# Kernel tuning notes

Hardware: AMD Instinct MI355X
Metric: run time of the kernel (lower is better)

The kernel has to match this reference:

```python
import math
import jax, jax.numpy as jnp
import numpy as np

B, N, D = 4, 1024, 512
HEADS, K = 8, 3
DH = D // HEADS
SMAX, SMIN, ALPHA_S = 0.2, 0.8, 3.0


def setup_inputs() -> dict:
    key = jax.random.key(0)
    ks = jax.random.split(key, 6)
    X = jax.random.normal(ks[0], (B, N, D), dtype=jnp.float32)
    # per-head GraphConstructor temperature (init 1.0 in torch)
    temperature = jnp.ones((HEADS,), dtype=jnp.float32)
    # per-head, per-hop filter weights: [HEADS, K+1, DH, DH]
    W_filt = jax.random.normal(ks[1], (HEADS, K + 1, DH, DH), dtype=jnp.float32) / math.sqrt(DH)
    # per-head hop mixing coefficients (random so output is non-trivial)
    alpha = jax.random.normal(ks[2], (HEADS, K + 1), dtype=jnp.float32) * 0.5
    W_proj = jax.random.normal(ks[3], (D, D), dtype=jnp.float32) / math.sqrt(D)
    b_proj = jnp.zeros((D,), dtype=jnp.float32)
    return {"X": X, "temperature": temperature, "W_filt": W_filt, "alpha": alpha,
            "W_proj": W_proj, "b_proj": b_proj, "layer_idx": 1, "L": 4}


def reference(X, temperature, W_filt, alpha, W_proj, b_proj, layer_idx, L):
    b, n, d = X.shape
    Xh = X.reshape(b, n, HEADS, DH).transpose(0, 2, 1, 3)  # [B,H,N,DH]

    # sparsity schedule -> static top-k size
    sparsity = SMIN + (SMAX - SMIN) * math.exp(-ALPHA_S * layer_idx / L)
    k_val = max(1, int((1.0 - sparsity) * n))

    tau = jnp.clip(temperature, 0.1, 5.0)  # [H]
    scale = math.sqrt(DH)
    # per-head attention scores: [B,H,N,N]
    S = jnp.einsum('bhnd,bhmd->bhnm', Xh, Xh) / (scale * tau[None, :, None, None])

    if k_val < n:
        thresh = jax.lax.top_k(S, k_val)[0][..., -1:]  # k-th largest per row
        S = jnp.where(S < thresh, -jnp.inf, S)
    A = jax.nn.softmax(S, axis=-1)  # row-stochastic sparse-pattern adjacency

    # K-hop polynomial filter, all heads at once
    P = Xh
    H = alpha[None, :, 0, None, None] * jnp.einsum('bhnd,hde->bhne', P, W_filt[:, 0])
    for k in range(1, K + 1):
        P = jnp.einsum('bhnm,bhmd->bhnd', A, P)
        H = H + alpha[None, :, k, None, None] * jnp.einsum('bhnd,hde->bhne', P, W_filt[:, k])

    out = H.transpose(0, 2, 1, 3).reshape(b, n, d)  # concat heads
    return out @ W_proj.T + b_proj
```

## Files before the change

### kernel.cpp

```cpp
#include <hip/hip_runtime.h>
#include <math.h>

#define Nq   1024
#define Dq   512
#define Hq   8
#define KH   3
#define DHq  64
#define NBH  32

typedef __attribute__((ext_vector_type(8))) __bf16 bf16x8;
typedef __attribute__((ext_vector_type(4))) float f32x4;

#define LDA 136
#define LDW 72


__device__ __forceinline__ unsigned short f2bf(float f) {
    unsigned int u = __float_as_uint(f);
    u += 0x7FFFu + ((u >> 16) & 1u);
    return (unsigned short)(u >> 16);
}
__device__ __forceinline__ float bf2f(unsigned short b) {
    return __uint_as_float(((unsigned int)b) << 16);
}
__device__ __forceinline__ unsigned key16(unsigned int b) {
    return (b & 0x8000u) ? (0xFFFFu & ~b) : (b | 0x8000u);
}
__device__ __forceinline__ uint2 pack4(float4 v) {
    return make_uint2((unsigned)f2bf(v.x) | ((unsigned)f2bf(v.y) << 16),
                      (unsigned)f2bf(v.z) | ((unsigned)f2bf(v.w) << 16));
}
__device__ __forceinline__ f32x4 fzero() { f32x4 z = {0.f, 0.f, 0.f, 0.f}; return z; }



__global__ __launch_bounds__(256) void xcast_kernel(const float* __restrict__ X,
                                                    unsigned short* __restrict__ Xn,
                                                    unsigned short* __restrict__ Xt) {
    __shared__ float T[64][68];
    int tid = threadIdx.x;
    int bh = blockIdx.y, b = bh >> 3, h = bh & 7;
    int n0 = blockIdx.x << 6;
    const float* Xg = X + ((size_t)b * Nq + n0) * Dq + h * DHq;
#pragma unroll
    for (int u = 0; u < 4; ++u) {
        int idx = tid + (u << 8);
        int r = idx >> 4, c4 = (idx & 15) << 2;
        float4 v = *(const float4*)&Xg[(size_t)r * Dq + c4];
        *(uint2*)&Xn[((size_t)bh * Nq + n0 + r) * DHq + c4] = pack4(v);
        T[c4 + 0][r] = v.x; T[c4 + 1][r] = v.y; T[c4 + 2][r] = v.z; T[c4 + 3][r] = v.w;
    }
    __syncthreads();
#pragma unroll
    for (int u = 0; u < 4; ++u) {
        int idx = tid + (u << 8);
        int d = idx >> 4, n4 = (idx & 15) << 2;
        float4 v = make_float4(T[d][n4], T[d][n4 + 1], T[d][n4 + 2], T[d][n4 + 3]);
        *(uint2*)&Xt[((size_t)bh * DHq + d) * Nq + n0 + n4] = pack4(v);
    }
}

__global__ __launch_bounds__(256) void score_mfma(const unsigned short* __restrict__ Xn,
                                                  const float* __restrict__ temperature,
                                                  unsigned short* __restrict__ Sbf) {
    __shared__ unsigned short Xi[64 * LDW], Xj[64 * LDW];
    int tid = threadIdx.x, lane = tid & 63, w = tid >> 6;
    int bh = blockIdx.z, i0 = blockIdx.y << 6, j0 = blockIdx.x << 6;
    const unsigned short* Xb = Xn + (size_t)bh * Nq * DHq;
    {
        int row = tid >> 3, o = (tid & 7) << 3;
#pragma unroll
        for (int u = 0; u < 2; ++u) {
            int r = row + (u << 5);
            *(uint4*)&Xi[r * LDW + o] = *(const uint4*)&Xb[(size_t)(i0 + r) * DHq + o];
            *(uint4*)&Xj[r * LDW + o] = *(const uint4*)&Xb[(size_t)(j0 + r) * DHq + o];
        }
    }
    __syncthreads();
    f32x4 acc[4] = {fzero(), fzero(), fzero(), fzero()};
    int brow = lane & 15, ko = (lane >> 4) << 3;
    const unsigned short* Afr = &Xi[((w << 4) + brow) * LDW + ko];
#pragma unroll
    for (int ks = 0; ks < 2; ++ks) {
        bf16x8 af = *(const bf16x8*)(Afr + (ks << 5));
#pragma unroll
        for (int nt = 0; nt < 4; ++nt) {
            bf16x8 bfv = *(const bf16x8*)&Xj[((nt << 4) + brow) * LDW + (ks << 5) + ko];
            acc[nt] = __builtin_amdgcn_mfma_f32_16x16x32_bf16(af, bfv, acc[nt], 0, 0, 0);
        }
    }
    float tau = fminf(fmaxf(temperature[bh & 7], 0.1f), 5.0f);
    float inv = 1.0f / (8.0f * tau);
    int nrow = (w << 4) + ((lane >> 4) << 2);
    unsigned short* Sp = Sbf + ((size_t)bh * Nq + i0 + nrow) * Nq + j0;
#pragma unroll
    for (int nt = 0; nt < 4; ++nt)
#pragma unroll
        for (int r = 0; r < 4; ++r)
            Sp[(size_t)r * Nq + (nt << 4) + brow] = f2bf(acc[nt][r] * inv);
}

__global__ __launch_bounds__(256) void topk_softmax_kernel(unsigned short* __restrict__ Sbf,
                                                           const int* __restrict__ layer_idx,
                                                           const int* __restrict__ Lptr) {
    int tid = threadIdx.x;
    int w = tid >> 6, lane = tid & 63;
    unsigned short* Srow = Sbf + ((size_t)blockIdx.x * 4 + w) * Nq;
    uint4 q0 = ((const uint4*)Srow)[lane * 2];
    uint4 q1 = ((const uint4*)Srow)[lane * 2 + 1];
    float v[16]; unsigned int k16[16];
    {
        unsigned int ww[8] = {q0.x, q0.y, q0.z, q0.w, q1.x, q1.y, q1.z, q1.w};
#pragma unroll
        for (int i = 0; i < 8; ++i) {
            unsigned lo16 = ww[i] & 0xFFFFu, hi16 = ww[i] >> 16;
            v[2 * i]     = __uint_as_float(lo16 << 16);
            v[2 * i + 1] = __uint_as_float(hi16 << 16);
            k16[2 * i]     = key16(lo16);
            k16[2 * i + 1] = key16(hi16);
        }
    }

    double sp = 0.8 + (0.2 - 0.8) * exp(-3.0 * (double)layer_idx[0] / (double)Lptr[0]);
    int kv = (int)((1.0 - sp) * (double)Nq);
    if (kv < 1) kv = 1;

    unsigned int tk = 0;
    if (kv < Nq) {
        unsigned int lo = 0;
#pragma unroll
        for (int bit = 15; bit >= 0; --bit) {
            unsigned int t = lo | (1u << bit);
            int cnt = 0;
#pragma unroll
            for (int i = 0; i < 16; ++i)
                cnt += (int)__popcll(__ballot(k16[i] >= t));
            if (cnt >= kv) lo = t;
        }
        tk = lo;
    }

    float m = v[0];
#pragma unroll
    for (int i = 1; i < 16; ++i) m = fmaxf(m, v[i]);
#pragma unroll
    for (int off = 32; off; off >>= 1) m = fmaxf(m, __shfl_xor(m, off));
    float sum = 0.f;
#pragma unroll
    for (int i = 0; i < 16; ++i) {
        float e = (k16[i] >= tk) ? __expf(v[i] - m) : 0.0f;
        v[i] = e; sum += e;
    }
#pragma unroll
    for (int off = 32; off; off >>= 1) sum += __shfl_xor(sum, off);
    float inv = 1.0f / sum;
    unsigned int ow[8];
#pragma unroll
    for (int i = 0; i < 8; ++i)
        ow[i] = (unsigned)f2bf(v[2 * i] * inv) | ((unsigned)f2bf(v[2 * i + 1] * inv) << 16);
    ((uint4*)Srow)[lane * 2]     = make_uint4(ow[0], ow[1], ow[2], ow[3]);
    ((uint4*)Srow)[lane * 2 + 1] = make_uint4(ow[4], ow[5], ow[6], ow[7]);
}

__global__ __launch_bounds__(256) void filt0_mfma(const unsigned short* __restrict__ Xn,
                                                  const float* __restrict__ W_filt,
                                                  const float* __restrict__ alpha,
                                                  float* __restrict__ Hacc) {
    __shared__ unsigned short PnL[64 * LDW], WtL[64 * LDW];
    int tid = threadIdx.x, lane = tid & 63, w = tid >> 6;
    int bh = blockIdx.y, b = bh >> 3, h = bh & 7;
    int n0 = blockIdx.x << 6;
    {
        int row = tid >> 3, o = (tid & 7) << 3;
        const unsigned short* Xb = Xn + ((size_t)bh * Nq + n0) * DHq;
#pragma unroll
        for (int u = 0; u < 2; ++u) {
            int r = row + (u << 5);
            *(uint4*)&PnL[r * LDW + o] = *(const uint4*)&Xb[(size_t)r * DHq + o];
        }
    }
    const float* Wg = W_filt + (size_t)h * (KH + 1) * DHq * DHq;
    for (int u = tid; u < 1024; u += 256) {
        int d = u >> 4, e4 = (u & 15) << 2;
        float4 wv = *(const float4*)&Wg[d * 64 + e4];
        WtL[(e4 + 0) * LDW + d] = f2bf(wv.x);
        WtL[(e4 + 1) * LDW + d] = f2bf(wv.y);
        WtL[(e4 + 2) * LDW + d] = f2bf(wv.z);
        WtL[(e4 + 3) * LDW + d] = f2bf(wv.w);
    }
    __syncthreads();
    f32x4 acc[4] = {fzero(), fzero(), fzero(), fzero()};
    int brow = lane & 15, ko = (lane >> 4) << 3;
    const unsigned short* Afr = &PnL[((w << 4) + brow) * LDW + ko];
#pragma unroll
    for (int ks = 0; ks < 2; ++ks) {
        bf16x8 af = *(const bf16x8*)(Afr + (ks << 5));
#pragma unroll
        for (int nt = 0; nt < 4; ++nt) {
            bf16x8 bfv = *(const bf16x8*)&WtL[((nt << 4) + brow) * LDW + (ks << 5) + ko];
            acc[nt] = __builtin_amdgcn_mfma_f32_16x16x32_bf16(af, bfv, acc[nt], 0, 0, 0);
        }
    }
    float av = alpha[h * (KH + 1)];
    int nrow = (w << 4) + ((lane >> 4) << 2);
    float* Ho = Hacc + ((size_t)b * Nq + n0 + nrow) * Dq + h * DHq;
#pragma unroll
    for (int nt = 0; nt < 4; ++nt)
#pragma unroll
        for (int r = 0; r < 4; ++r)
            Ho[(size_t)r * Dq + (nt << 4) + brow] = av * acc[nt][r];
}

__global__ __launch_bounds__(256) void apf_mfma(const unsigned short* __restrict__ Abf,
                                                const unsigned short* __restrict__ Ptin,
                                                unsigned short* __restrict__ Ptout, int writeP,
                                                const float* __restrict__ W_filt,
                                                const float* __restrict__ alpha,
                                                float* __restrict__ Hacc, int khop) {
    __shared__ unsigned short A_lds[2][64 * LDA];
    __shared__ unsigned short P_lds[2][64 * LDA];
    int tid = threadIdx.x, lane = tid & 63, w = tid >> 6;
    int bh = blockIdx.y, b = bh >> 3, h = bh & 7;
    int n0 = blockIdx.x << 6;
    const unsigned short* Ag = Abf + ((size_t)bh * Nq + n0) * Nq;
    const unsigned short* Pg = Ptin + (size_t)bh * DHq * Nq;
    int r0 = tid >> 4, oo = (tid & 15) << 3;

    uint4 ra[4], rp[4];
#pragma unroll
    for (int u = 0; u < 4; ++u) {
        ra[u] = *(const uint4*)&Ag[(size_t)(r0 + (u << 4)) * Nq + oo];
        rp[u] = *(const uint4*)&Pg[(size_t)(r0 + (u << 4)) * Nq + oo];
    }
#pragma unroll
    for (int u = 0; u < 4; ++u) {
        *(uint4*)&A_lds[0][(r0 + (u << 4)) * LDA + oo] = ra[u];
        *(uint4*)&P_lds[0][(r0 + (u << 4)) * LDA + oo] = rp[u];
    }
    __syncthreads();

    f32x4 acc[4] = {fzero(), fzero(), fzero(), fzero()};
    int brow = lane & 15, ko = (lane >> 4) << 3;
    int cur = 0;

    for (int kt = 0; kt < 8; ++kt) {
        if (kt < 7) {
            int j = (kt + 1) << 7;
#pragma unroll
            for (int u = 0; u < 4; ++u) {
                ra[u] = *(const uint4*)&Ag[(size_t)(r0 + (u << 4)) * Nq + j + oo];
                rp[u] = *(const uint4*)&Pg[(size_t)(r0 + (u << 4)) * Nq + j + oo];
            }
        }
        const unsigned short* Afr = &A_lds[cur][((w << 4) + brow) * LDA + ko];
#pragma unroll
        for (int ks = 0; ks < 4; ++ks) {
            bf16x8 af = *(const bf16x8*)(Afr + (ks << 5));
#pragma unroll
            for (int nt = 0; nt < 4; ++nt) {
                bf16x8 bfv = *(const bf16x8*)&P_lds[cur][((nt << 4) + brow) * LDA + (ks << 5) + ko];
                acc[nt] = __builtin_amdgcn_mfma_f32_16x16x32_bf16(af, bfv, acc[nt], 0, 0, 0);
            }
        }
        if (kt < 7) {
#pragma unroll
            for (int u = 0; u < 4; ++u) {
                *(uint4*)&A_lds[cur ^ 1][(r0 + (u << 4)) * LDA + oo] = ra[u];
                *(uint4*)&P_lds[cur ^ 1][(r0 + (u << 4)) * LDA + oo] = rp[u];
            }
        }
        __syncthreads();
        cur ^= 1;
    }

    int nrow = (w << 4) + ((lane >> 4) << 2);
    int dcol = lane & 15;
    if (writeP) {
#pragma unroll
        for (int nt = 0; nt < 4; ++nt) {
            uint2 pk = make_uint2(
                (unsigned)f2bf(acc[nt][0]) | ((unsigned)f2bf(acc[nt][1]) << 16),
                (unsigned)f2bf(acc[nt][2]) | ((unsigned)f2bf(acc[nt][3]) << 16));
            *(uint2*)&Ptout[(size_t)bh * DHq * Nq + (size_t)((nt << 4) + dcol) * Nq + n0 + nrow] = pk;
        }
    }
    unsigned short* PnL = &A_lds[0][0];
    unsigned short* WtL = &P_lds[0][0];
#pragma unroll
    for (int nt = 0; nt < 4; ++nt)
#pragma unroll
        for (int r = 0; r < 4; ++r)
            PnL[(nrow + r) * LDW + (nt << 4) + dcol] = f2bf(acc[nt][r]);
    const float* Wg = W_filt + ((size_t)h * (KH + 1) + khop) * DHq * DHq;
    for (int u = tid; u < 1024; u += 256) {
        int d = u >> 4, e4 = (u & 15) << 2;
        float4 wv = *(const float4*)&Wg[d * 64 + e4];
        WtL[(e4 + 0) * LDW + d] = f2bf(wv.x);
        WtL[(e4 + 1) * LDW + d] = f2bf(wv.y);
        WtL[(e4 + 2) * LDW + d] = f2bf(wv.z);
        WtL[(e4 + 3) * LDW + d] = f2bf(wv.w);
    }
    __syncthreads();
    f32x4 hacc[4] = {fzero(), fzero(), fzero(), fzero()};
    const unsigned short* Pfr = &PnL[((w << 4) + brow) * LDW + ko];
#pragma unroll
    for (int ks = 0; ks < 2; ++ks) {
        bf16x8 af = *(const bf16x8*)(Pfr + (ks << 5));
#pragma unroll
        for (int nt = 0; nt < 4; ++nt) {
            bf16x8 bfv = *(const bf16x8*)&WtL[((nt << 4) + brow) * LDW + (ks << 5) + ko];
            hacc[nt] = __builtin_amdgcn_mfma_f32_16x16x32_bf16(af, bfv, hacc[nt], 0, 0, 0);
        }
    }
    float av = alpha[h * (KH + 1) + khop];
    float* Ho = Hacc + ((size_t)b * Nq + n0 + nrow) * Dq + h * DHq;
#pragma unroll
    for (int nt = 0; nt < 4; ++nt)
#pragma unroll
        for (int r = 0; r < 4; ++r) {
            float* p = Ho + (size_t)r * Dq + (nt << 4) + dcol;
            *p += av * hacc[nt][r];
        }
}

__global__ __launch_bounds__(256) void proj_mfma(const float* __restrict__ Hacc,
                                                 const float* __restrict__ Wp,
                                                 const float* __restrict__ bp,
                                                 float* __restrict__ out) {
    __shared__ unsigned short Hl[64 * LDA], Wl[64 * LDA];
    int tid = threadIdx.x, lane = tid & 63, w = tid >> 6;
    int i0 = blockIdx.y << 6, j0 = blockIdx.x << 6;
    f32x4 acc[4] = {fzero(), fzero(), fzero(), fzero()};
    int brow = lane & 15, ko = (lane >> 4) << 3;
    for (int kt = 0; kt < 4; ++kt) {
#pragma unroll
        for (int u = 0; u < 8; ++u) {
            int c = tid + (u << 8);
            int r = c >> 5, o4 = (c & 31) << 2;
            float4 hv = *(const float4*)&Hacc[(size_t)(i0 + r) * Dq + (kt << 7) + o4];
            *(uint2*)&Hl[r * LDA + o4] = pack4(hv);
            float4 wv = *(const float4*)&Wp[(size_t)(j0 + r) * Dq + (kt << 7) + o4];
            *(uint2*)&Wl[r * LDA + o4] = pack4(wv);
        }
        __syncthreads();
        const unsigned short* Afr = &Hl[((w << 4) + brow) * LDA + ko];
#pragma unroll
        for (int ks = 0; ks < 4; ++ks) {
            bf16x8 af = *(const bf16x8*)(Afr + (ks << 5));
#pragma unroll
            for (int nt = 0; nt < 4; ++nt) {
                bf16x8 bfv = *(const bf16x8*)&Wl[((nt << 4) + brow) * LDA + (ks << 5) + ko];
                acc[nt] = __builtin_amdgcn_mfma_f32_16x16x32_bf16(af, bfv, acc[nt], 0, 0, 0);
            }
        }
        __syncthreads();
    }
    int nrow = (w << 4) + ((lane >> 4) << 2);
#pragma unroll
    for (int nt = 0; nt < 4; ++nt) {
        float bb = bp[j0 + (nt << 4) + brow];
#pragma unroll
        for (int r = 0; r < 4; ++r)
            out[(size_t)(i0 + nrow + r) * Dq + j0 + (nt << 4) + brow] = acc[nt][r] + bb;
    }
}


extern "C" void kernel_launch(void* const* d_in, const int* in_sizes, int n_in,
                              void* d_out, int out_size, void* d_ws, size_t ws_size,
                              hipStream_t stream) {
    (void)in_sizes; (void)n_in; (void)out_size; (void)ws_size;
    const float* X           = (const float*)d_in[0];
    const float* temperature = (const float*)d_in[1];
    const float* W_filt      = (const float*)d_in[2];
    const float* alpha       = (const float*)d_in[3];
    const float* W_proj      = (const float*)d_in[4];
    const float* b_proj      = (const float*)d_in[5];
    const int*   layer_idx   = (const int*)d_in[6];
    const int*   Lp          = (const int*)d_in[7];
    float* out = (float*)d_out;

    unsigned short* Sbf = (unsigned short*)d_ws;
    unsigned short* Xn  = Sbf + (size_t)NBH * Nq * Nq;
    unsigned short* Xt  = Xn  + (size_t)NBH * Nq * DHq;
    unsigned short* Pt1 = Xt  + (size_t)NBH * DHq * Nq;
    unsigned short* Pt2 = Pt1 + (size_t)NBH * DHq * Nq;
    float* Hacc = (float*)(Pt2 + (size_t)NBH * DHq * Nq);

    dim3 blk(256);
    xcast_kernel<<<dim3(16, 32), blk, 0, stream>>>(X, Xn, Xt);
    score_mfma<<<dim3(16, 16, 32), blk, 0, stream>>>(Xn, temperature, Sbf);
    topk_softmax_kernel<<<dim3(NBH * Nq / 4), blk, 0, stream>>>(Sbf, layer_idx, Lp);

    filt0_mfma<<<dim3(16, 32), blk, 0, stream>>>(Xn, W_filt, alpha, Hacc);
    apf_mfma<<<dim3(16, 32), blk, 0, stream>>>(Sbf, Xt, Pt1, 1, W_filt, alpha, Hacc, 1);
    apf_mfma<<<dim3(16, 32), blk, 0, stream>>>(Sbf, Pt1, Pt2, 1, W_filt, alpha, Hacc, 2);
    apf_mfma<<<dim3(16, 32), blk, 0, stream>>>(Sbf, Pt2, Pt1, 0, W_filt, alpha, Hacc, 3);

    proj_mfma<<<dim3(8, 64), blk, 0, stream>>>(Hacc, W_proj, b_proj, out);
}
```

Baseline: 224.8 us.

## Fuse score with top-k softmax, pre-cast weights, drop LDS staging in matmuls

Score computation and top-k/softmax are merged into one kernel that builds a 32-row score strip in shared memory, so the full bf16 score matrix is no longer written and re-read between kernels. The hop-0 filter is folded into the first hop kernel. Filter and projection weights are pre-converted to bf16 once in an extra block row of the cast kernel. The A·P and projection matmuls now read MFMA fragments straight from global memory instead of double-buffered LDS, and the H accumulator is stored as bf16, which adds rounding error across hops.

```diff
diff --git a/kernel.cpp b/kernel.cpp
--- a/kernel.cpp
+++ b/kernel.cpp
@@ -11,7 +11,7 @@
 typedef __attribute__((ext_vector_type(8))) __bf16 bf16x8;
 typedef __attribute__((ext_vector_type(4))) float f32x4;
 
-#define LDA 136
+#define SLS 1032
 #define LDW 72
 
 
@@ -36,9 +36,30 @@
 
 __global__ __launch_bounds__(256) void xcast_kernel(const float* __restrict__ X,
                                                     unsigned short* __restrict__ Xn,
-                                                    unsigned short* __restrict__ Xt) {
+                                                    unsigned short* __restrict__ Xt,
+                                                    const float* __restrict__ Wf,
+                                                    const float* __restrict__ Wp,
+                                                    unsigned short* __restrict__ WtB,
+                                                    unsigned short* __restrict__ WpB) {
+    int tid = threadIdx.x;
+    if (blockIdx.y == 32) {
+        int bx = blockIdx.x;
+#pragma unroll
+        for (int mm = 0; mm < 2; ++mm) {
+            int m = bx * 2 + mm;
+            for (int u = tid; u < 4096; u += 256) {
+                int d = u >> 6, e = u & 63;
+                WtB[m * 4096 + e * 64 + d] = f2bf(Wf[m * 4096 + d * 64 + e]);
+            }
+        }
+        for (int u = tid; u < 32 * 128; u += 256) {
+            int r = bx * 32 + (u >> 7), c4 = (u & 127) << 2;
+            float4 v = *(const float4*)&Wp[(size_t)r * Dq + c4];
+            *(uint2*)&WpB[(size_t)r * Dq + c4] = pack4(v);
+        }
+        return;
+    }
     __shared__ float T[64][68];
-    int tid = threadIdx.x;
     int bh = blockIdx.y, b = bh >> 3, h = bh & 7;
     int n0 = blockIdx.x << 6;
     const float* Xg = X + ((size_t)b * Nq + n0) * Dq + h * DHq;
@@ -60,302 +81,218 @@
     }
 }
 
-__global__ __launch_bounds__(256) void score_mfma(const unsigned short* __restrict__ Xn,
-                                                  const float* __restrict__ temperature,
-                                                  unsigned short* __restrict__ Sbf) {
-    __shared__ unsigned short Xi[64 * LDW], Xj[64 * LDW];
+__global__ __launch_bounds__(256) void score_topk_kernel(const unsigned short* __restrict__ Xn,
+                                                         const float* __restrict__ temperature,
+                                                         unsigned short* __restrict__ Abf,
+                                                         const int* __restrict__ layer_idx,
+                                                         const int* __restrict__ Lptr) {
+    __shared__ unsigned short strip[32 * SLS];
     int tid = threadIdx.x, lane = tid & 63, w = tid >> 6;
-    int bh = blockIdx.z, i0 = blockIdx.y << 6, j0 = blockIdx.x << 6;
+    int bh = blockIdx.y, i0 = blockIdx.x << 5;
+    int brow = lane & 15, g = lane >> 4, ko = g << 3;
     const unsigned short* Xb = Xn + (size_t)bh * Nq * DHq;
-    {
-        int row = tid >> 3, o = (tid & 7) << 3;
-#pragma unroll
-        for (int u = 0; u < 2; ++u) {
-            int r = row + (u << 5);
-            *(uint4*)&Xi[r * LDW + o] = *(const uint4*)&Xb[(size_t)(i0 + r) * DHq + o];
-            *(uint4*)&Xj[r * LDW + o] = *(const uint4*)&Xb[(size_t)(j0 + r) * DHq + o];
-        }
-    }
-    __syncthreads();
-    f32x4 acc[4] = {fzero(), fzero(), fzero(), fzero()};
-    int brow = lane & 15, ko = (lane >> 4) << 3;
-    const unsigned short* Afr = &Xi[((w << 4) + brow) * LDW + ko];
-#pragma unroll
-    for (int ks = 0; ks < 2; ++ks) {
-        bf16x8 af = *(const bf16x8*)(Afr + (ks << 5));
-#pragma unroll
-        for (int nt = 0; nt < 4; ++nt) {
-            bf16x8 bfv = *(const bf16x8*)&Xj[((nt << 4) + brow) * LDW + (ks << 5) + ko];
-            acc[nt] = __builtin_amdgcn_mfma_f32_16x16x32_bf16(af, bfv, acc[nt], 0, 0, 0);
-        }
-    }
+
+    int rows16 = (w >> 1) << 4, jhalf = w & 1;
+
+    bf16x8 af[2];
+#pragma unroll
+    for (int ks = 0; ks < 2; ++ks)
+        af[ks] = *(const bf16x8*)&Xb[(size_t)(i0 + rows16 + brow) * DHq + (ks << 5) + ko];
+
     float tau = fminf(fmaxf(temperature[bh & 7], 0.1f), 5.0f);
     float inv = 1.0f / (8.0f * tau);
-    int nrow = (w << 4) + ((lane >> 4) << 2);
-    unsigned short* Sp = Sbf + ((size_t)bh * Nq + i0 + nrow) * Nq + j0;
-#pragma unroll
-    for (int nt = 0; nt < 4; ++nt)
-#pragma unroll
-        for (int r = 0; r < 4; ++r)
-            Sp[(size_t)r * Nq + (nt << 4) + brow] = f2bf(acc[nt][r] * inv);
-}
-
-__global__ __launch_bounds__(256) void topk_softmax_kernel(unsigned short* __restrict__ Sbf,
-                                                           const int* __restrict__ layer_idx,
-                                                           const int* __restrict__ Lptr) {
-    int tid = threadIdx.x;
-    int w = tid >> 6, lane = tid & 63;
-    unsigned short* Srow = Sbf + ((size_t)blockIdx.x * 4 + w) * Nq;
-    uint4 q0 = ((const uint4*)Srow)[lane * 2];
-    uint4 q1 = ((const uint4*)Srow)[lane * 2 + 1];
-    float v[16]; unsigned int k16[16];
-    {
-        unsigned int ww[8] = {q0.x, q0.y, q0.z, q0.w, q1.x, q1.y, q1.z, q1.w};
-#pragma unroll
-        for (int i = 0; i < 8; ++i) {
-            unsigned lo16 = ww[i] & 0xFFFFu, hi16 = ww[i] >> 16;
-            v[2 * i]     = __uint_as_float(lo16 << 16);
-            v[2 * i + 1] = __uint_as_float(hi16 << 16);
-            k16[2 * i]     = key16(lo16);
-            k16[2 * i + 1] = key16(hi16);
-        }
-    }
+
+    for (int jc = 0; jc < 8; ++jc) {
+        int j0 = ((jhalf << 3) + jc) << 6;
+        f32x4 acc[4] = {fzero(), fzero(), fzero(), fzero()};
+#pragma unroll
+        for (int ks = 0; ks < 2; ++ks) {
+#pragma unroll
+            for (int nt = 0; nt < 4; ++nt) {
+                bf16x8 bfv = *(const bf16x8*)&Xb[(size_t)(j0 + (nt << 4) + brow) * DHq + (ks << 5) + ko];
+                acc[nt] = __builtin_amdgcn_mfma_f32_16x16x32_bf16(af[ks], bfv, acc[nt], 0, 0, 0);
+            }
+        }
+#pragma unroll
+        for (int nt = 0; nt < 4; ++nt)
+#pragma unroll
+            for (int r = 0; r < 4; ++r)
+                strip[(rows16 + (g << 2) + r) * SLS + j0 + (nt << 4) + brow] = f2bf(acc[nt][r] * inv);
+    }
+    __syncthreads();
 
     double sp = 0.8 + (0.2 - 0.8) * exp(-3.0 * (double)layer_idx[0] / (double)Lptr[0]);
     int kv = (int)((1.0 - sp) * (double)Nq);
     if (kv < 1) kv = 1;
 
-    unsigned int tk = 0;
-    if (kv < Nq) {
-        unsigned int lo = 0;
-#pragma unroll
-        for (int bit = 15; bit >= 0; --bit) {
-            unsigned int t = lo | (1u << bit);
-            int cnt = 0;
-#pragma unroll
-            for (int i = 0; i < 16; ++i)
-                cnt += (int)__popcll(__ballot(k16[i] >= t));
-            if (cnt >= kv) lo = t;
-        }
-        tk = lo;
-    }
-
-    float m = v[0];
-#pragma unroll
-    for (int i = 1; i < 16; ++i) m = fmaxf(m, v[i]);
-#pragma unroll
-    for (int off = 32; off; off >>= 1) m = fmaxf(m, __shfl_xor(m, off));
-    float sum = 0.f;
-#pragma unroll
-    for (int i = 0; i < 16; ++i) {
-        float e = (k16[i] >= tk) ? __expf(v[i] - m) : 0.0f;
-        v[i] = e; sum += e;
-    }
-#pragma unroll
-    for (int off = 32; off; off >>= 1) sum += __shfl_xor(sum, off);
-    float inv = 1.0f / sum;
-    unsigned int ow[8];
-#pragma unroll
-    for (int i = 0; i < 8; ++i)
-        ow[i] = (unsigned)f2bf(v[2 * i] * inv) | ((unsigned)f2bf(v[2 * i + 1] * inv) << 16);
-    ((uint4*)Srow)[lane * 2]     = make_uint4(ow[0], ow[1], ow[2], ow[3]);
-    ((uint4*)Srow)[lane * 2 + 1] = make_uint4(ow[4], ow[5], ow[6], ow[7]);
-}
-
-__global__ __launch_bounds__(256) void filt0_mfma(const unsigned short* __restrict__ Xn,
-                                                  const float* __restrict__ W_filt,
-                                                  const float* __restrict__ alpha,
-                                                  float* __restrict__ Hacc) {
-    __shared__ unsigned short PnL[64 * LDW], WtL[64 * LDW];
-    int tid = threadIdx.x, lane = tid & 63, w = tid >> 6;
-    int bh = blockIdx.y, b = bh >> 3, h = bh & 7;
-    int n0 = blockIdx.x << 6;
-    {
-        int row = tid >> 3, o = (tid & 7) << 3;
-        const unsigned short* Xb = Xn + ((size_t)bh * Nq + n0) * DHq;
-#pragma unroll
-        for (int u = 0; u < 2; ++u) {
-            int r = row + (u << 5);
-            *(uint4*)&PnL[r * LDW + o] = *(const uint4*)&Xb[(size_t)r * DHq + o];
-        }
-    }
-    const float* Wg = W_filt + (size_t)h * (KH + 1) * DHq * DHq;
-    for (int u = tid; u < 1024; u += 256) {
-        int d = u >> 4, e4 = (u & 15) << 2;
-        float4 wv = *(const float4*)&Wg[d * 64 + e4];
-        WtL[(e4 + 0) * LDW + d] = f2bf(wv.x);
-        WtL[(e4 + 1) * LDW + d] = f2bf(wv.y);
-        WtL[(e4 + 2) * LDW + d] = f2bf(wv.z);
-        WtL[(e4 + 3) * LDW + d] = f2bf(wv.w);
-    }
-    __syncthreads();
-    f32x4 acc[4] = {fzero(), fzero(), fzero(), fzero()};
-    int brow = lane & 15, ko = (lane >> 4) << 3;
-    const unsigned short* Afr = &PnL[((w << 4) + brow) * LDW + ko];
-#pragma unroll
-    for (int ks = 0; ks < 2; ++ks) {
-        bf16x8 af = *(const bf16x8*)(Afr + (ks << 5));
-#pragma unroll
-        for (int nt = 0; nt < 4; ++nt) {
-            bf16x8 bfv = *(const bf16x8*)&WtL[((nt << 4) + brow) * LDW + (ks << 5) + ko];
-            acc[nt] = __builtin_amdgcn_mfma_f32_16x16x32_bf16(af, bfv, acc[nt], 0, 0, 0);
-        }
-    }
-    float av = alpha[h * (KH + 1)];
-    int nrow = (w << 4) + ((lane >> 4) << 2);
-    float* Ho = Hacc + ((size_t)b * Nq + n0 + nrow) * Dq + h * DHq;
-#pragma unroll
-    for (int nt = 0; nt < 4; ++nt)
-#pragma unroll
-        for (int r = 0; r < 4; ++r)
-            Ho[(size_t)r * Dq + (nt << 4) + brow] = av * acc[nt][r];
+    for (int rr = 0; rr < 8; ++rr) {
+        int row = (w << 3) + rr;
+        const unsigned short* sp16 = &strip[row * SLS + lane * 16];
+        uint4 q0 = *(const uint4*)sp16;
+        uint4 q1 = *(const uint4*)(sp16 + 8);
+        float v[16]; unsigned int k16[16];
+        {
+            unsigned int ww[8] = {q0.x, q0.y, q0.z, q0.w, q1.x, q1.y, q1.z, q1.w};
+#pragma unroll
+            for (int i = 0; i < 8; ++i) {
+                unsigned lo16 = ww[i] & 0xFFFFu, hi16 = ww[i] >> 16;
+                v[2 * i]       = __uint_as_float(lo16 << 16);
+                v[2 * i + 1]   = __uint_as_float(hi16 << 16);
+                k16[2 * i]     = key16(lo16);
+                k16[2 * i + 1] = key16(hi16);
+            }
+        }
+        unsigned int tk = 0;
+        if (kv < Nq) {
+            unsigned int lo = 0;
+#pragma unroll
+            for (int bit = 15; bit >= 0; --bit) {
+                unsigned int t = lo | (1u << bit);
+                int cnt = 0;
+#pragma unroll
+                for (int i = 0; i < 16; ++i)
+                    cnt += (int)__popcll(__ballot(k16[i] >= t));
+                if (cnt >= kv) lo = t;
+            }
+            tk = lo;
+        }
+        float m = v[0];
+#pragma unroll
+        for (int i = 1; i < 16; ++i) m = fmaxf(m, v[i]);
+#pragma unroll
+        for (int off = 32; off; off >>= 1) m = fmaxf(m, __shfl_xor(m, off));
+        float sum = 0.f;
+#pragma unroll
+        for (int i = 0; i < 16; ++i) {
+            float e = (k16[i] >= tk) ? __expf(v[i] - m) : 0.0f;
+            v[i] = e; sum += e;
+        }
+#pragma unroll
+        for (int off = 32; off; off >>= 1) sum += __shfl_xor(sum, off);
+        float is = 1.0f / sum;
+        unsigned int ow[8];
+#pragma unroll
+        for (int i = 0; i < 8; ++i)
+            ow[i] = (unsigned)f2bf(v[2 * i] * is) | ((unsigned)f2bf(v[2 * i + 1] * is) << 16);
+        unsigned short* Ar = Abf + ((size_t)bh * Nq + i0 + row) * Nq + lane * 16;
+        *(uint4*)Ar       = make_uint4(ow[0], ow[1], ow[2], ow[3]);
+        *(uint4*)(Ar + 8) = make_uint4(ow[4], ow[5], ow[6], ow[7]);
+    }
 }
 
 __global__ __launch_bounds__(256) void apf_mfma(const unsigned short* __restrict__ Abf,
                                                 const unsigned short* __restrict__ Ptin,
                                                 unsigned short* __restrict__ Ptout, int writeP,
-                                                const float* __restrict__ W_filt,
+                                                const unsigned short* __restrict__ Xn,
+                                                const unsigned short* __restrict__ WtB,
                                                 const float* __restrict__ alpha,
-                                                float* __restrict__ Hacc, int khop) {
-    __shared__ unsigned short A_lds[2][64 * LDA];
-    __shared__ unsigned short P_lds[2][64 * LDA];
+                                                unsigned short* __restrict__ HaccB, int khop) {
+    __shared__ unsigned short PnL[64 * LDW];
     int tid = threadIdx.x, lane = tid & 63, w = tid >> 6;
     int bh = blockIdx.y, b = bh >> 3, h = bh & 7;
-    int n0 = blockIdx.x << 6;
-    const unsigned short* Ag = Abf + ((size_t)bh * Nq + n0) * Nq;
+    int i0 = blockIdx.x << 6;
+    int brow = lane & 15, g = lane >> 4, ko = g << 3;
+    const unsigned short* Ag = Abf + ((size_t)bh * Nq + i0) * Nq;
     const unsigned short* Pg = Ptin + (size_t)bh * DHq * Nq;
-    int r0 = tid >> 4, oo = (tid & 15) << 3;
-
-    uint4 ra[4], rp[4];
-#pragma unroll
-    for (int u = 0; u < 4; ++u) {
-        ra[u] = *(const uint4*)&Ag[(size_t)(r0 + (u << 4)) * Nq + oo];
-        rp[u] = *(const uint4*)&Pg[(size_t)(r0 + (u << 4)) * Nq + oo];
-    }
-#pragma unroll
-    for (int u = 0; u < 4; ++u) {
-        *(uint4*)&A_lds[0][(r0 + (u << 4)) * LDA + oo] = ra[u];
-        *(uint4*)&P_lds[0][(r0 + (u << 4)) * LDA + oo] = rp[u];
-    }
-    __syncthreads();
 
     f32x4 acc[4] = {fzero(), fzero(), fzero(), fzero()};
-    int brow = lane & 15, ko = (lane >> 4) << 3;
-    int cur = 0;
-
+    int arow = (w << 4) + brow;
     for (int kt = 0; kt < 8; ++kt) {
-        if (kt < 7) {
-            int j = (kt + 1) << 7;
-#pragma unroll
-            for (int u = 0; u < 4; ++u) {
-                ra[u] = *(const uint4*)&Ag[(size_t)(r0 + (u << 4)) * Nq + j + oo];
-                rp[u] = *(const uint4*)&Pg[(size_t)(r0 + (u << 4)) * Nq + j + oo];
-            }
-        }
-        const unsigned short* Afr = &A_lds[cur][((w << 4) + brow) * LDA + ko];
 #pragma unroll
         for (int ks = 0; ks < 4; ++ks) {
-            bf16x8 af = *(const bf16x8*)(Afr + (ks << 5));
+            int kg = (kt << 7) + (ks << 5) + ko;
+            bf16x8 af = *(const bf16x8*)&Ag[(size_t)arow * Nq + kg];
 #pragma unroll
             for (int nt = 0; nt < 4; ++nt) {
-                bf16x8 bfv = *(const bf16x8*)&P_lds[cur][((nt << 4) + brow) * LDA + (ks << 5) + ko];
+                bf16x8 bfv = *(const bf16x8*)&Pg[(size_t)((nt << 4) + brow) * Nq + kg];
                 acc[nt] = __builtin_amdgcn_mfma_f32_16x16x32_bf16(af, bfv, acc[nt], 0, 0, 0);
             }
         }
-        if (kt < 7) {
-#pragma unroll
-            for (int u = 0; u < 4; ++u) {
-                *(uint4*)&A_lds[cur ^ 1][(r0 + (u << 4)) * LDA + oo] = ra[u];
-                *(uint4*)&P_lds[cur ^ 1][(r0 + (u << 4)) * LDA + oo] = rp[u];
-            }
-        }
-        __syncthreads();
-        cur ^= 1;
-    }
-
-    int nrow = (w << 4) + ((lane >> 4) << 2);
-    int dcol = lane & 15;
+    }
+
+    int nrow = (w << 4) + (g << 2);
     if (writeP) {
 #pragma unroll
         for (int nt = 0; nt < 4; ++nt) {
             uint2 pk = make_uint2(
                 (unsigned)f2bf(acc[nt][0]) | ((unsigned)f2bf(acc[nt][1]) << 16),
                 (unsigned)f2bf(acc[nt][2]) | ((unsigned)f2bf(acc[nt][3]) << 16));
-            *(uint2*)&Ptout[(size_t)bh * DHq * Nq + (size_t)((nt << 4) + dcol) * Nq + n0 + nrow] = pk;
-        }
-    }
-    unsigned short* PnL = &A_lds[0][0];
-    unsigned short* WtL = &P_lds[0][0];
+            *(uint2*)&Ptout[(size_t)bh * DHq * Nq + (size_t)((nt << 4) + brow) * Nq + i0 + nrow] = pk;
+        }
+    }
 #pragma unroll
     for (int nt = 0; nt < 4; ++nt)
 #pragma unroll
         for (int r = 0; r < 4; ++r)
-            PnL[(nrow + r) * LDW + (nt << 4) + dcol] = f2bf(acc[nt][r]);
-    const float* Wg = W_filt + ((size_t)h * (KH + 1) + khop) * DHq * DHq;
-    for (int u = tid; u < 1024; u += 256) {
-        int d = u >> 4, e4 = (u & 15) << 2;
-        float4 wv = *(const float4*)&Wg[d * 64 + e4];
-        WtL[(e4 + 0) * LDW + d] = f2bf(wv.x);
-        WtL[(e4 + 1) * LDW + d] = f2bf(wv.y);
-        WtL[(e4 + 2) * LDW + d] = f2bf(wv.z);
-        WtL[(e4 + 3) * LDW + d] = f2bf(wv.w);
-    }
-    __syncthreads();
+            PnL[(nrow + r) * LDW + (nt << 4) + brow] = f2bf(acc[nt][r]);
+
+    const unsigned short* Wk = WtB + (size_t)(h * (KH + 1) + khop) * DHq * DHq;
     f32x4 hacc[4] = {fzero(), fzero(), fzero(), fzero()};
-    const unsigned short* Pfr = &PnL[((w << 4) + brow) * LDW + ko];
+    f32x4 hacc0[4] = {fzero(), fzero(), fzero(), fzero()};
 #pragma unroll
     for (int ks = 0; ks < 2; ++ks) {
-        bf16x8 af = *(const bf16x8*)(Pfr + (ks << 5));
+        bf16x8 pf = *(const bf16x8*)&PnL[((w << 4) + brow) * LDW + (ks << 5) + ko];
 #pragma unroll
         for (int nt = 0; nt < 4; ++nt) {
-            bf16x8 bfv = *(const bf16x8*)&WtL[((nt << 4) + brow) * LDW + (ks << 5) + ko];
-            hacc[nt] = __builtin_amdgcn_mfma_f32_16x16x32_bf16(af, bfv, hacc[nt], 0, 0, 0);
+            bf16x8 wf = *(const bf16x8*)&Wk[(size_t)((nt << 4) + brow) * DHq + (ks << 5) + ko];
+            hacc[nt] = __builtin_amdgcn_mfma_f32_16x16x32_bf16(pf, wf, hacc[nt], 0, 0, 0);
+        }
+    }
+    if (khop == 1) {
+        const unsigned short* W0 = WtB + (size_t)(h * (KH + 1)) * DHq * DHq;
+        const unsigned short* Xb = Xn + ((size_t)bh * Nq + i0) * DHq;
+#pragma unroll
+        for (int ks = 0; ks < 2; ++ks) {
+            bf16x8 xf = *(const bf16x8*)&Xb[(size_t)arow * DHq + (ks << 5) + ko];
+#pragma unroll
+            for (int nt = 0; nt < 4; ++nt) {
+                bf16x8 wf = *(const bf16x8*)&W0[(size_t)((nt << 4) + brow) * DHq + (ks << 5) + ko];
+                hacc0[nt] = __builtin_amdgcn_mfma_f32_16x16x32_bf16(xf, wf, hacc0[nt], 0, 0, 0);
+            }
         }
     }
     float av = alpha[h * (KH + 1) + khop];
-    float* Ho = Hacc + ((size_t)b * Nq + n0 + nrow) * Dq + h * DHq;
-#pragma unroll
-    for (int nt = 0; nt < 4; ++nt)
-#pragma unroll
-        for (int r = 0; r < 4; ++r) {
-            float* p = Ho + (size_t)r * Dq + (nt << 4) + dcol;
-            *p += av * hacc[nt][r];
-        }
-}
-
-__global__ __launch_bounds__(256) void proj_mfma(const float* __restrict__ Hacc,
-                                                 const float* __restrict__ Wp,
+    unsigned short* Ho = HaccB + ((size_t)b * Nq + i0 + nrow) * Dq + h * DHq;
+    if (khop == 1) {
+        float a0 = alpha[h * (KH + 1)];
+#pragma unroll
+        for (int nt = 0; nt < 4; ++nt)
+#pragma unroll
+            for (int r = 0; r < 4; ++r)
+                Ho[(size_t)r * Dq + (nt << 4) + brow] = f2bf(a0 * hacc0[nt][r] + av * hacc[nt][r]);
+    } else {
+#pragma unroll
+        for (int nt = 0; nt < 4; ++nt)
+#pragma unroll
+            for (int r = 0; r < 4; ++r) {
+                unsigned short* p = Ho + (size_t)r * Dq + (nt << 4) + brow;
+                *p = f2bf(bf2f(*p) + av * hacc[nt][r]);
+            }
+    }
+}
+
+__global__ __launch_bounds__(256) void proj_mfma(const unsigned short* __restrict__ HaccB,
+                                                 const unsigned short* __restrict__ WpB,
                                                  const float* __restrict__ bp,
                                                  float* __restrict__ out) {
-    __shared__ unsigned short Hl[64 * LDA], Wl[64 * LDA];
     int tid = threadIdx.x, lane = tid & 63, w = tid >> 6;
     int i0 = blockIdx.y << 6, j0 = blockIdx.x << 6;
+    int brow = lane & 15, g = lane >> 4, ko = g << 3;
     f32x4 acc[4] = {fzero(), fzero(), fzero(), fzero()};
-    int brow = lane & 15, ko = (lane >> 4) << 3;
+    int arow = i0 + (w << 4) + brow;
     for (int kt = 0; kt < 4; ++kt) {
 #pragma unroll
-        for (int u = 0; u < 8; ++u) {
-            int c = tid + (u << 8);
-            int r = c >> 5, o4 = (c & 31) << 2;
-            float4 hv = *(const float4*)&Hacc[(size_t)(i0 + r) * Dq + (kt << 7) + o4];
-            *(uint2*)&Hl[r * LDA + o4] = pack4(hv);
-            float4 wv = *(const float4*)&Wp[(size_t)(j0 + r) * Dq + (kt << 7) + o4];
-            *(uint2*)&Wl[r * LDA + o4] = pack4(wv);
-        }
-        __syncthreads();
-        const unsigned short* Afr = &Hl[((w << 4) + brow) * LDA + ko];
-#pragma unroll
         for (int ks = 0; ks < 4; ++ks) {
-            bf16x8 af = *(const bf16x8*)(Afr + (ks << 5));
+            int kg = (kt << 7) + (ks << 5) + ko;
+            bf16x8 af = *(const bf16x8*)&HaccB[(size_t)arow * Dq + kg];
 #pragma unroll
             for (int nt = 0; nt < 4; ++nt) {
-                bf16x8 bfv = *(const bf16x8*)&Wl[((nt << 4) + brow) * LDA + (ks << 5) + ko];
+                bf16x8 bfv = *(const bf16x8*)&WpB[(size_t)(j0 + (nt << 4) + brow) * Dq + kg];
                 acc[nt] = __builtin_amdgcn_mfma_f32_16x16x32_bf16(af, bfv, acc[nt], 0, 0, 0);
             }
         }
-        __syncthreads();
-    }
-    int nrow = (w << 4) + ((lane >> 4) << 2);
+    }
+    int nrow = (w << 4) + (g << 2);
 #pragma unroll
     for (int nt = 0; nt < 4; ++nt) {
         float bb = bp[j0 + (nt << 4) + brow];
@@ -380,22 +317,21 @@
     const int*   Lp          = (const int*)d_in[7];
     float* out = (float*)d_out;
 
-    unsigned short* Sbf = (unsigned short*)d_ws;
-    unsigned short* Xn  = Sbf + (size_t)NBH * Nq * Nq;
-    unsigned short* Xt  = Xn  + (size_t)NBH * Nq * DHq;
-    unsigned short* Pt1 = Xt  + (size_t)NBH * DHq * Nq;
-    unsigned short* Pt2 = Pt1 + (size_t)NBH * DHq * Nq;
-    float* Hacc = (float*)(Pt2 + (size_t)NBH * DHq * Nq);
+    unsigned short* Abf  = (unsigned short*)d_ws;
+    unsigned short* Xn   = Abf  + (size_t)NBH * Nq * Nq;
+    unsigned short* Xt   = Xn   + (size_t)NBH * Nq * DHq;
+    unsigned short* Pt1  = Xt   + (size_t)NBH * DHq * Nq;
+    unsigned short* Pt2  = Pt1  + (size_t)NBH * DHq * Nq;
+    unsigned short* Hacc = Pt2  + (size_t)NBH * DHq * Nq;
+    unsigned short* WtB  = Hacc + (size_t)4 * Nq * Dq;
+    unsigned short* WpB  = WtB  + (size_t)NBH * DHq * DHq;
 
     dim3 blk(256);
-    xcast_kernel<<<dim3(16, 32), blk, 0, stream>>>(X, Xn, Xt);
-    score_mfma<<<dim3(16, 16, 32), blk, 0, stream>>>(Xn, temperature, Sbf);
-    topk_softmax_kernel<<<dim3(NBH * Nq / 4), blk, 0, stream>>>(Sbf, layer_idx, Lp);
-
-    filt0_mfma<<<dim3(16, 32), blk, 0, stream>>>(Xn, W_filt, alpha, Hacc);
-    apf_mfma<<<dim3(16, 32), blk, 0, stream>>>(Sbf, Xt, Pt1, 1, W_filt, alpha, Hacc, 1);
-    apf_mfma<<<dim3(16, 32), blk, 0, stream>>>(Sbf, Pt1, Pt2, 1, W_filt, alpha, Hacc, 2);
-    apf_mfma<<<dim3(16, 32), blk, 0, stream>>>(Sbf, Pt2, Pt1, 0, W_filt, alpha, Hacc, 3);
-
-    proj_mfma<<<dim3(8, 64), blk, 0, stream>>>(Hacc, W_proj, b_proj, out);
-}
+    xcast_kernel<<<dim3(16, 33), blk, 0, stream>>>(X, Xn, Xt, W_filt, W_proj, WtB, WpB);
+    score_topk_kernel<<<dim3(32, 32), blk, 0, stream>>>(Xn, temperature, Abf, layer_idx, Lp);
+    apf_mfma<<<dim3(16, 32), blk, 0, stream>>>(Abf, Xt, Pt1, 1, Xn, WtB, alpha, Hacc, 1);
+    apf_mfma<<<dim3(16, 32), blk, 0, stream>>>(Abf, Pt1, Pt2, 1, Xn, WtB, alpha, Hacc, 2);
+    apf_mfma<<<dim3(16, 32), blk, 0, stream>>>(Abf, Pt2, nullptr, 0, Xn, WtB, alpha, Hacc, 3);
+
+    proj_mfma<<<dim3(8, 64), blk, 0, stream>>>(Hacc, WpB, b_proj, out);
+}
```

New measurement: 335.4 us. 49.2% more time.
